# Performance work log

Hardware: AMD Instinct MI355X
Metric: run time of the kernel (lower is better)

## Reference

```python
import jax, jax.numpy as jnp
import numpy as np

# Module config (init_kwargs)
OUT_H, OUT_W = 7, 7
SPATIAL_SCALE = 0.25
SAMPLE_NUM = 2          # fixed sampling grid (sample_num > 0 branch of mmcv kernel)
ALIGNED = True
CLOCKWISE = False

B, C, H, W = 2, 256, 200, 200
R = 1000


def setup_inputs() -> dict:
    key = jax.random.key(0)
    k1, k2, k3, k4, k5, k6 = jax.random.split(key, 6)
    features = jax.random.normal(k1, (B, C, H, W), dtype=jnp.float32)
    # rois: (batch_index, cx, cy, w, h, angle) in input-image coordinates
    bidx = jax.random.randint(k2, (R,), 0, B).astype(jnp.float32)
    cx = jax.random.uniform(k3, (R,), minval=100.0, maxval=700.0)
    cy = jax.random.uniform(k4, (R,), minval=100.0, maxval=700.0)
    wh = jax.random.uniform(k5, (R, 2), minval=20.0, maxval=200.0)
    ang = jax.random.uniform(k6, (R,), minval=-np.pi, maxval=np.pi)
    rois = jnp.concatenate(
        [bidx[:, None], cx[:, None], cy[:, None], wh, ang[:, None]], axis=1
    ).astype(jnp.float32)
    return {"features": features, "rois": rois}


def _bilinear_gather(features, bidx, y, x):
    """features: [B,C,H,W]; bidx: [R] int; y,x: [R,P] float. Returns [R,P,C]."""
    Hf, Wf = features.shape[2], features.shape[3]
    valid = (y > -1.0) & (y < Hf) & (x > -1.0) & (x < Wf)
    y = jnp.maximum(y, 0.0)
    x = jnp.maximum(x, 0.0)
    yl = jnp.floor(y).astype(jnp.int32)
    xl = jnp.floor(x).astype(jnp.int32)
    ych = yl >= Hf - 1
    xch = xl >= Wf - 1
    yl = jnp.where(ych, Hf - 1, yl)
    yh = jnp.where(ych, Hf - 1, yl + 1)
    xl = jnp.where(xch, Wf - 1, xl)
    xh = jnp.where(xch, Wf - 1, xl + 1)
    ly = jnp.where(ych, 0.0, y - yl.astype(y.dtype))
    lx = jnp.where(xch, 0.0, x - xl.astype(x.dtype))
    hy, hx = 1.0 - ly, 1.0 - lx
    b = bidx[:, None]  # [R,1] broadcast against [R,P]
    v1 = features[b, :, yl, xl]  # [R,P,C]
    v2 = features[b, :, yl, xh]
    v3 = features[b, :, yh, xl]
    v4 = features[b, :, yh, xh]
    val = (hy * hx)[..., None] * v1 + (hy * lx)[..., None] * v2 \
        + (ly * hx)[..., None] * v3 + (ly * lx)[..., None] * v4
    return jnp.where(valid[..., None], val, 0.0)


def _roi_align_rotated(features, rois):
    g = SAMPLE_NUM
    offset = 0.5 if ALIGNED else 0.0
    bidx = rois[:, 0].astype(jnp.int32)
    cx = rois[:, 1] * SPATIAL_SCALE - offset
    cy = rois[:, 2] * SPATIAL_SCALE - offset
    rw = rois[:, 3] * SPATIAL_SCALE
    rh = rois[:, 4] * SPATIAL_SCALE
    theta = -rois[:, 5] if CLOCKWISE else rois[:, 5]
    if not ALIGNED:
        rw = jnp.maximum(rw, 1.0)
        rh = jnp.maximum(rh, 1.0)
    bin_h = rh / OUT_H
    bin_w = rw / OUT_W
    # sample offsets within roi frame, origin at roi center
    ph = jnp.arange(OUT_H, dtype=jnp.float32)
    pw = jnp.arange(OUT_W, dtype=jnp.float32)
    ig = (jnp.arange(g, dtype=jnp.float32) + 0.5) / g
    # yy: [R, OUT_H, g]; xx: [R, OUT_W, g]
    yy = -rh[:, None, None] / 2.0 + (ph[None, :, None] + ig[None, None, :]) * bin_h[:, None, None]
    xx = -rw[:, None, None] / 2.0 + (pw[None, :, None] + ig[None, None, :]) * bin_w[:, None, None]
    # broadcast to [R, OUT_H, OUT_W, g, g]
    yy5 = yy[:, :, None, :, None]
    xx5 = xx[:, None, :, None, :]
    sin_t = jnp.sin(theta)[:, None, None, None, None]
    cos_t = jnp.cos(theta)[:, None, None, None, None]
    x = yy5 * sin_t + xx5 * cos_t + cx[:, None, None, None, None]
    y = yy5 * cos_t - xx5 * sin_t + cy[:, None, None, None, None]
    P = OUT_H * OUT_W * g * g
    vals = _bilinear_gather(features, bidx, y.reshape(R, P), x.reshape(R, P))  # [R,P,C]
    vals = vals.reshape(R, OUT_H, OUT_W, g * g, C).mean(axis=3)  # [R,OUT_H,OUT_W,C]
    return jnp.transpose(vals, (0, 3, 1, 2))  # [R,C,OUT_H,OUT_W]


def reference(features, rois):
    return _roi_align_rotated(features, rois)
```

## Files before the change

kernel.cpp:

```cpp
#include <hip/hip_runtime.h>
#include <math.h>

#define OUT_H 7
#define OUT_W 7
#define GS 2
#define NBINS (OUT_H * OUT_W)
#define NSAMP (GS * GS)
#define SPATIAL_SCALE 0.25f
#define B_ 2
#define C_ 256
#define H_ 200
#define W_ 200
#define R_ 1000
#define HW_ (H_ * W_)
#define NBMAX 13

typedef _Float16 half_t;
typedef __attribute__((ext_vector_type(8))) _Float16 half8;
typedef __attribute__((ext_vector_type(2))) _Float16 half2_t;
typedef __attribute__((ext_vector_type(4))) float f32x4;


__global__ __launch_bounds__(256)
void nchw_to_nhwc_h(const float* __restrict__ in, half_t* __restrict__ out,
                    const float* __restrict__ rois, int* __restrict__ perm) {
    __shared__ float tile[64][64];

    __shared__ int cnt[8];
    __shared__ int novf, take;
    __shared__ unsigned char claimed[R_];
    __shared__ short ovf[R_];
    if (blockIdx.x == 0 && blockIdx.y == 0 && blockIdx.z == 0) {
        const int t0 = threadIdx.x;
        if (t0 < 8) cnt[t0] = 0;
        if (t0 == 0) { novf = 0; take = 0; }
        for (int t = t0; t < R_; t += 256) claimed[t] = 0;
        __syncthreads();
        for (int t = t0; t < R_; t += 256) {
            const float* roi = rois + t * 6;
            int   b   = (int)roi[0];
            float cyf = roi[2] * SPATIAL_SCALE;
            int q = (int)((cyf - 25.0f) * (4.0f / 150.0f));
            q = q < 0 ? 0 : (q > 3 ? 3 : q);
            int band = b * 4 + q;
            band = band < 0 ? 0 : (band > 7 ? 7 : band);
            int rank = atomicAdd(&cnt[band], 1);
            if (rank < R_ / 8) {
                int id = band + 8 * rank;
                perm[id] = t;
                claimed[id] = 1;
            } else {
                ovf[atomicAdd(&novf, 1)] = (short)t;
            }
        }
        __syncthreads();
        for (int t = t0; t < R_; t += 256) {
            if (!claimed[t]) perm[t] = (int)ovf[atomicAdd(&take, 1)];
        }
    }

    const int hw0 = blockIdx.x * 64;
    const int c0  = blockIdx.y * 64;
    const int b   = blockIdx.z;
    const int t   = threadIdx.x;

    {
        const f32x4* ip4 = (const f32x4*)(in + ((size_t)b * C_ + c0) * HW_ + hw0);
        const int r = t >> 4;
        const int q = t & 15;
#pragma unroll
        for (int k = 0; k < 4; ++k) {
            const int c = r + 16 * k;
            f32x4 v = __builtin_nontemporal_load(&ip4[(size_t)c * (HW_ / 4) + q]);
            const int g = q ^ ((c ^ (c >> 3)) & 7);
            ((f32x4*)tile)[c * 16 + g] = v;
        }
    }
    __syncthreads();
    {
        const int cg = t & 7;
        const int hb = t >> 3;
        half_t* op = out + ((size_t)b * HW_ + hw0) * C_ + c0 + 8 * cg;
#pragma unroll
        for (int i = 0; i < 2; ++i) {
            const int hw = hb + 32 * i;
            const int gh = hw >> 2, oh = hw & 3;
            half8 h;
#pragma unroll
            for (int dc = 0; dc < 8; ++dc) {
                const int c = 8 * cg + dc;
                const float f = tile[c][4 * (gh ^ ((c ^ (c >> 3)) & 7)) + oh];
                h[dc] = (half_t)f;
            }
            *(half8*)(op + (size_t)hw * C_) = h;
        }
    }
}

__device__ __forceinline__ void mix2(float& a0, float& a1,
                                     unsigned int pair, float w) {
    asm("v_fma_mix_f32 %0, %1, %2, %0 op_sel:[0,0,0] op_sel_hi:[1,0,0]"
        : "+v"(a0) : "v"(pair), "v"(w));
    asm("v_fma_mix_f32 %0, %1, %2, %0 op_sel:[1,0,0] op_sel_hi:[1,0,0]"
        : "+v"(a1) : "v"(pair), "v"(w));
}

template<int NB>
__device__ __forceinline__ void gather_body(
        const uint2* __restrict__ fpu, int B0,
        const int4* __restrict__ s_o, const float4* __restrict__ s_w,
        int wave, int lane, int tid,
        float (&obuf)[4][64][NBMAX], float* __restrict__ out_r) {

    for (int j = wave; j < NB; j += 4) {
        const int m = j * NSAMP;
        const int4   o0 = s_o[m + 0], o1 = s_o[m + 1], o2 = s_o[m + 2], o3 = s_o[m + 3];
        const float4 w0 = s_w[m + 0], w1 = s_w[m + 1], w2 = s_w[m + 2], w3 = s_w[m + 3];

        const uint2 t0  = fpu[o0.x + lane];
        const uint2 t1  = fpu[o0.y + lane];
        const uint2 t2  = fpu[o0.z + lane];
        const uint2 t3  = fpu[o0.w + lane];
        const uint2 t4  = fpu[o1.x + lane];
        const uint2 t5  = fpu[o1.y + lane];
        const uint2 t6  = fpu[o1.z + lane];
        const uint2 t7  = fpu[o1.w + lane];
        const uint2 t8  = fpu[o2.x + lane];
        const uint2 t9  = fpu[o2.y + lane];
        const uint2 t10 = fpu[o2.z + lane];
        const uint2 t11 = fpu[o2.w + lane];
        const uint2 t12 = fpu[o3.x + lane];
        const uint2 t13 = fpu[o3.y + lane];
        const uint2 t14 = fpu[o3.z + lane];
        const uint2 t15 = fpu[o3.w + lane];

        float ax = 0.0f, ay = 0.0f, az = 0.0f, aw = 0.0f;

        mix2(ax, ay, t0.x,  w0.x); mix2(az, aw, t0.y,  w0.x);
        mix2(ax, ay, t1.x,  w0.y); mix2(az, aw, t1.y,  w0.y);
        mix2(ax, ay, t2.x,  w0.z); mix2(az, aw, t2.y,  w0.z);
        mix2(ax, ay, t3.x,  w0.w); mix2(az, aw, t3.y,  w0.w);

        mix2(ax, ay, t4.x,  w1.x); mix2(az, aw, t4.y,  w1.x);
        mix2(ax, ay, t5.x,  w1.y); mix2(az, aw, t5.y,  w1.y);
        mix2(ax, ay, t6.x,  w1.z); mix2(az, aw, t6.y,  w1.z);
        mix2(ax, ay, t7.x,  w1.w); mix2(az, aw, t7.y,  w1.w);

        mix2(ax, ay, t8.x,  w2.x); mix2(az, aw, t8.y,  w2.x);
        mix2(ax, ay, t9.x,  w2.y); mix2(az, aw, t9.y,  w2.y);
        mix2(ax, ay, t10.x, w2.z); mix2(az, aw, t10.y, w2.z);
        mix2(ax, ay, t11.x, w2.w); mix2(az, aw, t11.y, w2.w);

        mix2(ax, ay, t12.x, w3.x); mix2(az, aw, t12.y, w3.x);
        mix2(ax, ay, t13.x, w3.y); mix2(az, aw, t13.y, w3.y);
        mix2(ax, ay, t14.x, w3.z); mix2(az, aw, t14.y, w3.z);
        mix2(ax, ay, t15.x, w3.w); mix2(az, aw, t15.y, w3.w);

        obuf[0][lane][j] = ax;
        obuf[1][lane][j] = ay;
        obuf[2][lane][j] = az;
        obuf[3][lane][j] = aw;
    }
    __syncthreads();

    const int E = C_ * NB;
    for (int e = tid; e < E; e += 256) {
        const int c = e / NB;
        const int j = e - c * NB;
        out_r[(size_t)c * NBINS + B0 + j] = obuf[c & 3][c >> 2][j];
    }
}

__global__ __launch_bounds__(256, 6)
void gather_nhwc(const half_t* __restrict__ nhwc,
                 const float* __restrict__ rois,
                 const int* __restrict__ perm,
                 float* __restrict__ out) {
    __shared__ float  obuf[4][64][NBMAX];
    __shared__ int4   s_o[NBMAX * NSAMP];
    __shared__ float4 s_w[NBMAX * NSAMP];

    const int bid  = blockIdx.x;
    const int q    = bid / 1000;
    const int slot = bid - q * 1000;
    const int r    = perm[slot];
    const int NB   = (q == 3) ? 13 : 12;
    const int B0   = 12 * q;

    const int tid  = threadIdx.x;
    const int wave = tid >> 6;
    const int lane = tid & 63;

    if (tid < NB * NSAMP) {
        const float* roi = rois + r * 6;
        const int   b     = (int)roi[0];
        const float cx    = roi[1] * SPATIAL_SCALE - 0.5f;
        const float cy    = roi[2] * SPATIAL_SCALE - 0.5f;
        const float rw    = roi[3] * SPATIAL_SCALE;
        const float rh    = roi[4] * SPATIAL_SCALE;
        const float theta = roi[5];
        const float bin_h = rh * (1.0f / OUT_H);
        const float bin_w = rw * (1.0f / OUT_W);
        float st, ct;
        __sincosf(theta, &st, &ct);

        const int bin = B0 + (tid >> 2);
        const int s   = tid & 3;
        const int ph  = bin / OUT_W, pw = bin % OUT_W;
        const int iy  = s >> 1,      ix = s & 1;

        const float yy = -rh * 0.5f + ((float)ph + ((float)iy + 0.5f) * 0.5f) * bin_h;
        const float xx = -rw * 0.5f + ((float)pw + ((float)ix + 0.5f) * 0.5f) * bin_w;
        float x = yy * st + xx * ct + cx;
        float y = yy * ct - xx * st + cy;

        const bool valid = (y > -1.0f) && (y < (float)H_) &&
                           (x > -1.0f) && (x < (float)W_);
        y = fmaxf(y, 0.0f);
        x = fmaxf(x, 0.0f);
        int yl = (int)y, xl = (int)x;
        int yh; float ly;
        if (yl >= H_ - 1) { yl = H_ - 1; yh = H_ - 1; ly = 0.0f; }
        else              { yh = yl + 1; ly = y - (float)yl; }
        int xh; float lx;
        if (xl >= W_ - 1) { xl = W_ - 1; xh = W_ - 1; lx = 0.0f; }
        else              { xh = xl + 1; lx = x - (float)xl; }
        const float hy = 1.0f - ly, hx = 1.0f - lx;
        const float scale = valid ? (1.0f / NSAMP) : 0.0f;

        const int bplane = b * HW_;
        s_o[tid] = make_int4((bplane + yl * W_ + xl) * (C_ / 4),
                             (bplane + yl * W_ + xh) * (C_ / 4),
                             (bplane + yh * W_ + xl) * (C_ / 4),
                             (bplane + yh * W_ + xh) * (C_ / 4));
        s_w[tid] = make_float4(hy * hx * scale, hy * lx * scale,
                               ly * hx * scale, ly * lx * scale);
    }
    __syncthreads();

    const uint2* __restrict__ fpu = (const uint2*)nhwc;
    float* out_r = out + (size_t)r * (C_ * NBINS);

    if (q == 3) gather_body<13>(fpu, B0, s_o, s_w, wave, lane, tid, obuf, out_r);
    else        gather_body<12>(fpu, B0, s_o, s_w, wave, lane, tid, obuf, out_r);
}


struct alignas(16) Samp {
    int o0, o1, o2, o3;
    float w0, w1, w2, w3;
};

__device__ __forceinline__ Samp compute_samp(const float* __restrict__ rois,
                                             int r, int ph, int pw, int s) {
    const float* roi = rois + r * 6;
    int   b     = (int)roi[0];
    float cx    = roi[1] * SPATIAL_SCALE - 0.5f;
    float cy    = roi[2] * SPATIAL_SCALE - 0.5f;
    float rw    = roi[3] * SPATIAL_SCALE;
    float rh    = roi[4] * SPATIAL_SCALE;
    float theta = roi[5];
    float bin_h = rh * (1.0f / OUT_H);
    float bin_w = rw * (1.0f / OUT_W);
    int iy = s / GS, ix = s % GS;
    float yy = -rh * 0.5f + ((float)ph + ((float)iy + 0.5f) * (1.0f / GS)) * bin_h;
    float xx = -rw * 0.5f + ((float)pw + ((float)ix + 0.5f) * (1.0f / GS)) * bin_w;
    float st = sinf(theta), ct = cosf(theta);
    float x = yy * st + xx * ct + cx;
    float y = yy * ct - xx * st + cy;
    bool valid = (y > -1.0f) && (y < (float)H_) && (x > -1.0f) && (x < (float)W_);
    y = fmaxf(y, 0.0f);
    x = fmaxf(x, 0.0f);
    int yl = (int)y;
    int xl = (int)x;
    int yh; float ly;
    if (yl >= H_ - 1) { yl = H_ - 1; yh = H_ - 1; ly = 0.0f; }
    else              { yh = yl + 1; ly = y - (float)yl; }
    int xh; float lx;
    if (xl >= W_ - 1) { xl = W_ - 1; xh = W_ - 1; lx = 0.0f; }
    else              { xh = xl + 1; lx = x - (float)xl; }
    float hy = 1.0f - ly, hx = 1.0f - lx;
    float scale = valid ? (1.0f / NSAMP) : 0.0f;
    Samp sp;
    int base = b * (C_ * H_ * W_);
    sp.o0 = base + yl * W_ + xl;
    sp.o1 = base + yl * W_ + xh;
    sp.o2 = base + yh * W_ + xl;
    sp.o3 = base + yh * W_ + xh;
    sp.w0 = hy * hx * scale;
    sp.w1 = hy * lx * scale;
    sp.w2 = ly * hx * scale;
    sp.w3 = ly * lx * scale;
    return sp;
}

__global__ __launch_bounds__(256)
void mono_kernel(const float* __restrict__ feat,
                 const float* __restrict__ rois,
                 float* __restrict__ out) {
    int tid = blockIdx.x * blockDim.x + threadIdx.x;
    if (tid >= R_ * C_ * NBINS) return;
    int bin = tid % NBINS;
    int rc  = tid / NBINS;
    int c   = rc % C_;
    int r   = rc / C_;
    int coff = c * (H_ * W_);
    float acc = 0.0f;
#pragma unroll
    for (int s = 0; s < NSAMP; ++s) {
        Samp t = compute_samp(rois, r, bin / OUT_W, bin % OUT_W, s);
        acc += t.w0 * feat[coff + t.o0];
        acc += t.w1 * feat[coff + t.o1];
        acc += t.w2 * feat[coff + t.o2];
        acc += t.w3 * feat[coff + t.o3];
    }
    out[tid] = acc;
}


extern "C" void kernel_launch(void* const* d_in, const int* in_sizes, int n_in,
                              void* d_out, int out_size, void* d_ws, size_t ws_size,
                              hipStream_t stream) {
    const float* feat = (const float*)d_in[0];
    const float* rois = (const float*)d_in[1];
    float* out = (float*)d_out;

    const size_t nhwc_bytes = (size_t)B_ * C_ * HW_ * sizeof(half_t);
    const size_t perm_bytes = (size_t)R_ * sizeof(int);

    if (ws_size >= nhwc_bytes + perm_bytes) {
        half_t* nhwc = (half_t*)d_ws;
        int*    perm = (int*)((char*)d_ws + nhwc_bytes);
        dim3 tgrid(HW_ / 64, C_ / 64, B_);
        nchw_to_nhwc_h<<<tgrid, 256, 0, stream>>>(feat, nhwc, rois, perm);
        gather_nhwc<<<4 * R_, 256, 0, stream>>>(nhwc, rois, perm, out);
    } else {
        const int n_out = R_ * C_ * NBINS;
        mono_kernel<<<(n_out + 255) / 256, 256, 0, stream>>>(feat, rois, out);
    }
}
```

Baseline: 174.6 us.

## Gather one whole ROI per 512-thread block with double-buffered tap loads

```diff
diff --git a/kernel.cpp b/kernel.cpp
--- a/kernel.cpp
+++ b/kernel.cpp
@@ -6,6 +6,7 @@
 #define GS 2
 #define NBINS (OUT_H * OUT_W)
 #define NSAMP (GS * GS)
+#define NMETA (NBINS * NSAMP)
 #define SPATIAL_SCALE 0.25f
 #define B_ 2
 #define C_ 256
@@ -13,7 +14,6 @@
 #define W_ 200
 #define R_ 1000
 #define HW_ (H_ * W_)
-#define NBMAX 13
 
 typedef _Float16 half_t;
 typedef __attribute__((ext_vector_type(8))) _Float16 half8;
@@ -105,93 +105,55 @@
         : "+v"(a1) : "v"(pair), "v"(w));
 }
 
-template<int NB>
-__device__ __forceinline__ void gather_body(
-        const uint2* __restrict__ fpu, int B0,
-        const int4* __restrict__ s_o, const float4* __restrict__ s_w,
-        int wave, int lane, int tid,
-        float (&obuf)[4][64][NBMAX], float* __restrict__ out_r) {
-
-    for (int j = wave; j < NB; j += 4) {
-        const int m = j * NSAMP;
-        const int4   o0 = s_o[m + 0], o1 = s_o[m + 1], o2 = s_o[m + 2], o3 = s_o[m + 3];
-        const float4 w0 = s_w[m + 0], w1 = s_w[m + 1], w2 = s_w[m + 2], w3 = s_w[m + 3];
-
-        const uint2 t0  = fpu[o0.x + lane];
-        const uint2 t1  = fpu[o0.y + lane];
-        const uint2 t2  = fpu[o0.z + lane];
-        const uint2 t3  = fpu[o0.w + lane];
-        const uint2 t4  = fpu[o1.x + lane];
-        const uint2 t5  = fpu[o1.y + lane];
-        const uint2 t6  = fpu[o1.z + lane];
-        const uint2 t7  = fpu[o1.w + lane];
-        const uint2 t8  = fpu[o2.x + lane];
-        const uint2 t9  = fpu[o2.y + lane];
-        const uint2 t10 = fpu[o2.z + lane];
-        const uint2 t11 = fpu[o2.w + lane];
-        const uint2 t12 = fpu[o3.x + lane];
-        const uint2 t13 = fpu[o3.y + lane];
-        const uint2 t14 = fpu[o3.z + lane];
-        const uint2 t15 = fpu[o3.w + lane];
-
-        float ax = 0.0f, ay = 0.0f, az = 0.0f, aw = 0.0f;
-
-        mix2(ax, ay, t0.x,  w0.x); mix2(az, aw, t0.y,  w0.x);
-        mix2(ax, ay, t1.x,  w0.y); mix2(az, aw, t1.y,  w0.y);
-        mix2(ax, ay, t2.x,  w0.z); mix2(az, aw, t2.y,  w0.z);
-        mix2(ax, ay, t3.x,  w0.w); mix2(az, aw, t3.y,  w0.w);
-
-        mix2(ax, ay, t4.x,  w1.x); mix2(az, aw, t4.y,  w1.x);
-        mix2(ax, ay, t5.x,  w1.y); mix2(az, aw, t5.y,  w1.y);
-        mix2(ax, ay, t6.x,  w1.z); mix2(az, aw, t6.y,  w1.z);
-        mix2(ax, ay, t7.x,  w1.w); mix2(az, aw, t7.y,  w1.w);
-
-        mix2(ax, ay, t8.x,  w2.x); mix2(az, aw, t8.y,  w2.x);
-        mix2(ax, ay, t9.x,  w2.y); mix2(az, aw, t9.y,  w2.y);
-        mix2(ax, ay, t10.x, w2.z); mix2(az, aw, t10.y, w2.z);
-        mix2(ax, ay, t11.x, w2.w); mix2(az, aw, t11.y, w2.w);
-
-        mix2(ax, ay, t12.x, w3.x); mix2(az, aw, t12.y, w3.x);
-        mix2(ax, ay, t13.x, w3.y); mix2(az, aw, t13.y, w3.y);
-        mix2(ax, ay, t14.x, w3.z); mix2(az, aw, t14.y, w3.z);
-        mix2(ax, ay, t15.x, w3.w); mix2(az, aw, t15.y, w3.w);
-
-        obuf[0][lane][j] = ax;
-        obuf[1][lane][j] = ay;
-        obuf[2][lane][j] = az;
-        obuf[3][lane][j] = aw;
-    }
-    __syncthreads();
-
-    const int E = C_ * NB;
-    for (int e = tid; e < E; e += 256) {
-        const int c = e / NB;
-        const int j = e - c * NB;
-        out_r[(size_t)c * NBINS + B0 + j] = obuf[c & 3][c >> 2][j];
-    }
-}
-
-__global__ __launch_bounds__(256, 6)
+struct Taps { uint2 t[16]; };
+
+__device__ __forceinline__ void load_taps(Taps& T, const uint2* __restrict__ fpu,
+                                          const int4* __restrict__ s_o,
+                                          int m, int lane) {
+#pragma unroll
+    for (int i = 0; i < 4; ++i) {
+        const int4 o = s_o[m + i];
+        T.t[4 * i + 0] = fpu[o.x + lane];
+        T.t[4 * i + 1] = fpu[o.y + lane];
+        T.t[4 * i + 2] = fpu[o.z + lane];
+        T.t[4 * i + 3] = fpu[o.w + lane];
+    }
+}
+
+__device__ __forceinline__ void fma_store(const Taps& T,
+                                          const float4* __restrict__ s_w,
+                                          int m, int j, int lane,
+                                          float (&obuf)[4][64][NBINS]) {
+    float ax = 0.0f, ay = 0.0f, az = 0.0f, aw = 0.0f;
+#pragma unroll
+    for (int i = 0; i < 4; ++i) {
+        const float4 w = s_w[m + i];
+        mix2(ax, ay, T.t[4 * i + 0].x, w.x); mix2(az, aw, T.t[4 * i + 0].y, w.x);
+        mix2(ax, ay, T.t[4 * i + 1].x, w.y); mix2(az, aw, T.t[4 * i + 1].y, w.y);
+        mix2(ax, ay, T.t[4 * i + 2].x, w.z); mix2(az, aw, T.t[4 * i + 2].y, w.z);
+        mix2(ax, ay, T.t[4 * i + 3].x, w.w); mix2(az, aw, T.t[4 * i + 3].y, w.w);
+    }
+    obuf[0][lane][j] = ax;
+    obuf[1][lane][j] = ay;
+    obuf[2][lane][j] = az;
+    obuf[3][lane][j] = aw;
+}
+
+__global__ __launch_bounds__(512, 4)
 void gather_nhwc(const half_t* __restrict__ nhwc,
                  const float* __restrict__ rois,
                  const int* __restrict__ perm,
                  float* __restrict__ out) {
-    __shared__ float  obuf[4][64][NBMAX];
-    __shared__ int4   s_o[NBMAX * NSAMP];
-    __shared__ float4 s_w[NBMAX * NSAMP];
-
-    const int bid  = blockIdx.x;
-    const int q    = bid / 1000;
-    const int slot = bid - q * 1000;
-    const int r    = perm[slot];
-    const int NB   = (q == 3) ? 13 : 12;
-    const int B0   = 12 * q;
-
+    __shared__ float  obuf[4][64][NBINS];
+    __shared__ int4   s_o[NMETA];
+    __shared__ float4 s_w[NMETA];
+
+    const int r    = perm[blockIdx.x];
     const int tid  = threadIdx.x;
     const int wave = tid >> 6;
     const int lane = tid & 63;
 
-    if (tid < NB * NSAMP) {
+    if (tid < NMETA) {
         const float* roi = rois + r * 6;
         const int   b     = (int)roi[0];
         const float cx    = roi[1] * SPATIAL_SCALE - 0.5f;
@@ -204,7 +166,7 @@
         float st, ct;
         __sincosf(theta, &st, &ct);
 
-        const int bin = B0 + (tid >> 2);
+        const int bin = tid >> 2;
         const int s   = tid & 3;
         const int ph  = bin / OUT_W, pw = bin % OUT_W;
         const int iy  = s >> 1,      ix = s & 1;
@@ -239,10 +201,43 @@
     __syncthreads();
 
     const uint2* __restrict__ fpu = (const uint2*)nhwc;
+
+    {
+        Taps A, B;
+        int j = wave;
+        load_taps(A, fpu, s_o, 4 * j, lane);
+        while (true) {
+            const int j2 = j + 8;
+            if (j2 < NBINS) {
+                load_taps(B, fpu, s_o, 4 * j2, lane);
+                fma_store(A, s_w, 4 * j, j, lane, obuf);
+                const int j3 = j2 + 8;
+                if (j3 < NBINS) {
+                    load_taps(A, fpu, s_o, 4 * j3, lane);
+                    fma_store(B, s_w, 4 * j2, j2, lane, obuf);
+                    j = j3;
+                    continue;
+                }
+                fma_store(B, s_w, 4 * j2, j2, lane, obuf);
+                break;
+            }
+            fma_store(A, s_w, 4 * j, j, lane, obuf);
+            break;
+        }
+    }
+    __syncthreads();
+
     float* out_r = out + (size_t)r * (C_ * NBINS);
-
-    if (q == 3) gather_body<13>(fpu, B0, s_o, s_w, wave, lane, tid, obuf, out_r);
-    else        gather_body<12>(fpu, B0, s_o, s_w, wave, lane, tid, obuf, out_r);
+    const int E = C_ * NBINS;
+#pragma unroll
+    for (int i = 0; i < (E + 511) / 512; ++i) {
+        const int f = tid + 512 * i;
+        if (f < E) {
+            const int c = f / NBINS;
+            const int j = f - c * NBINS;
+            __builtin_nontemporal_store(obuf[c & 3][c >> 2][j], &out_r[f]);
+        }
+    }
 }
 
 
@@ -333,7 +328,7 @@
         int*    perm = (int*)((char*)d_ws + nhwc_bytes);
         dim3 tgrid(HW_ / 64, C_ / 64, B_);
         nchw_to_nhwc_h<<<tgrid, 256, 0, stream>>>(feat, nhwc, rois, perm);
-        gather_nhwc<<<4 * R_, 256, 0, stream>>>(nhwc, rois, perm, out);
+        gather_nhwc<<<R_, 512, 0, stream>>>(nhwc, rois, perm, out);
     } else {
         const int n_out = R_ * C_ * NBINS;
         mono_kernel<<<(n_out + 255) / 256, 256, 0, stream>>>(feat, rois, out);
```

New measurement: 158.7 us. 9.1% less time.
